# Performance work log

Hardware: AMD Instinct MI355X
Metric: run time of the kernel (lower is better)

## Reference

```python
import jax, jax.numpy as jnp
import numpy as np

D_MODEL = 1024
N_HEAD = 16
D_H = D_MODEL // N_HEAD


def setup_inputs() -> dict:
    key = jax.random.key(0)
    ks = jax.random.split(key, 5)
    scale = 1.0 / np.sqrt(D_MODEL)
    x = jax.random.normal(ks[0], (4, 2048, D_MODEL), dtype=jnp.float32)
    # torch nn.Linear weights: shape (out_features, in_features)
    W_qkv = jax.random.uniform(ks[1], (3 * D_MODEL, D_MODEL), dtype=jnp.float32, minval=-scale, maxval=scale)
    b_qkv = jax.random.uniform(ks[2], (3 * D_MODEL,), dtype=jnp.float32, minval=-scale, maxval=scale)
    W_o = jax.random.uniform(ks[3], (D_MODEL, D_MODEL), dtype=jnp.float32, minval=-scale, maxval=scale)
    b_o = jax.random.uniform(ks[4], (D_MODEL,), dtype=jnp.float32, minval=-scale, maxval=scale)
    return {"x": x, "W_qkv": W_qkv, "b_qkv": b_qkv, "W_o": W_o, "b_o": b_o}


def reference(x, W_qkv, b_qkv, W_o, b_o):
    B, S, D = x.shape
    qkv = jnp.einsum('bsd,ed->bse', x, W_qkv) + b_qkv  # [B,S,3D]
    q, k, v = jnp.split(qkv, 3, axis=-1)
    # [B,H,S,d_h]
    q = q.reshape(B, S, N_HEAD, D_H).transpose(0, 2, 1, 3)
    k = k.reshape(B, S, N_HEAD, D_H).transpose(0, 2, 1, 3)
    v = v.reshape(B, S, N_HEAD, D_H).transpose(0, 2, 1, 3)
    sim = jnp.einsum('bhqd,bhkd->bhqk', q, k) / jnp.sqrt(jnp.float32(D_H))
    neg_inf = jnp.finfo(sim.dtype).min
    causal = jnp.tril(jnp.ones((S, S), dtype=bool))
    sim = jnp.where(causal[None, None], sim, neg_inf)
    attn = jax.nn.softmax(sim, axis=-1)
    out = jnp.einsum('bhqk,bhkd->bhqd', attn, v)  # [B,H,S,d_h]
    out = out.transpose(0, 2, 1, 3).reshape(B, S, D)
    return jnp.einsum('bsd,ed->bse', out, W_o) + b_o
```

## Files before the change

### kernel.cpp

```cpp
#include <hip/hip_runtime.h>

#define D_MODEL 1024
#define S_LEN   2048
#define BATCH   4
#define NH      16
#define DH      64
#define M_ROWS  (BATCH * S_LEN)

typedef __attribute__((ext_vector_type(8))) short short8;
typedef __attribute__((ext_vector_type(4))) float floatx4;
typedef unsigned short ushort_t;
typedef __attribute__((ext_vector_type(4))) ushort_t ushortx4;

__device__ __forceinline__ ushort_t f2bf(float f) {
    union { float f; unsigned u; } v; v.f = f;
    unsigned r = v.u + 0x7FFFu + ((v.u >> 16) & 1u);
    return (ushort_t)(r >> 16);
}

__device__ __forceinline__ int pack2(float lo, float hi) {
    return (int)__builtin_amdgcn_perm(__float_as_uint(hi), __float_as_uint(lo), 0x07060302u);
}

__device__ __forceinline__ void async_copy16(const ushort_t* g, ushort_t* l) {
    __builtin_amdgcn_global_load_lds(
        (const __attribute__((address_space(1))) void*)g,
        (__attribute__((address_space(3))) void*)l,
        16, 0, 0);
}

#define N0 (M_ROWS * D_MODEL)
#define N1 (3 * D_MODEL * D_MODEL)
#define N2 (D_MODEL * D_MODEL)
#define NQUADS ((N0 + N1 + N2) / 4)

__global__ __launch_bounds__(256)
void cvt_f32_bf16(const float* __restrict__ s0, const float* __restrict__ s1,
                  const float* __restrict__ s2, ushort_t* __restrict__ d0,
                  ushort_t* __restrict__ d1, ushort_t* __restrict__ d2)
{
    const int q = blockIdx.x * 256 + threadIdx.x;
    if (q >= NQUADS) return;
    const float* s; ushort_t* d; int e;
    if (q < N0 / 4)            { s = s0; d = d0; e = q * 4; }
    else if (q < (N0 + N1) / 4){ s = s1; d = d1; e = q * 4 - N0; }
    else                       { s = s2; d = d2; e = q * 4 - N0 - N1; }
    const float4 v = *(const float4*)&s[e];
    ushortx4 o;
    o[0] = f2bf(v.x); o[1] = f2bf(v.y); o[2] = f2bf(v.z); o[3] = f2bf(v.w);
    *(ushortx4*)&d[e] = o;
}

template<int BM, int BN, int NWAVES, int MINW, bool F32OUT, bool VSPLIT>
__global__ __launch_bounds__(NWAVES * 64, MINW)
void gemm_bt_bias(const ushort_t* __restrict__ A, const ushort_t* __restrict__ B,
                  const float* __restrict__ bias, void* __restrict__ Cv,
                  ushort_t* __restrict__ vt, int M, int N, int K)
{
    constexpr int BK = 64;
    constexpr int AI = BM / 8 / NWAVES;
    constexpr int BI = BN / 8 / NWAVES;
    constexpr float C2 = 0.18033688011112042f;
    __shared__ ushort_t As[BM][BK];
    __shared__ ushort_t Bs[BN][BK];

    const int tid  = threadIdx.x;
    const int lane = tid & 63;
    const int wave = tid >> 6;
    const int quad = lane >> 4;
    const int l16  = lane & 15;
    const int l8r  = lane >> 3;
    const int c8   = lane & 7;
    const int swz  = l16 & 7;

    const int gdx = gridDim.x;
    const int bid = blockIdx.y * gdx + blockIdx.x;
    const int nwg = gdx * gridDim.y;
    const int sw  = (bid & 7) * (nwg >> 3) + (bid >> 3);
    const int bm  = (sw / gdx) * BM;
    const int bn  = (sw % gdx) * BN;

    const int wm = (wave % (BM / 64)) * 64;
    const int wn = (wave / (BM / 64)) * 64;

    const ushort_t* ag[AI]; ushort_t* al[AI];
    const ushort_t* bg[BI]; ushort_t* bl[BI];
    #pragma unroll
    for (int i = 0; i < AI; i++) {
        const int ri = (wave + i * NWAVES) * 8;
        ag[i] = &A[(size_t)(bm + ri + l8r) * K + (c8 ^ l8r) * 8];
        al[i] = &As[ri][0];
    }
    #pragma unroll
    for (int i = 0; i < BI; i++) {
        const int ri = (wave + i * NWAVES) * 8;
        bg[i] = &B[(size_t)(bn + ri + l8r) * K + (c8 ^ l8r) * 8];
        bl[i] = &Bs[ri][0];
    }

    floatx4 acc[4][4] = {};

    for (int k0 = 0; k0 < K; k0 += BK) {
        __syncthreads();
        #pragma unroll
        for (int i = 0; i < AI; i++) async_copy16(ag[i] + k0, al[i]);
        #pragma unroll
        for (int i = 0; i < BI; i++) async_copy16(bg[i] + k0, bl[i]);
        __syncthreads();

        #pragma unroll
        for (int h = 0; h < 2; h++) {
            short8 af[4], bfr[4];
            #pragma unroll
            for (int i = 0; i < 4; i++)
                af[i]  = *(const short8*)&As[wm + i * 16 + l16][((h * 4 + quad) ^ swz) * 8];
            #pragma unroll
            for (int i = 0; i < 4; i++)
                bfr[i] = *(const short8*)&Bs[wn + i * 16 + l16][((h * 4 + quad) ^ swz) * 8];

            #pragma unroll
            for (int mi = 0; mi < 4; mi++)
                #pragma unroll
                for (int ni = 0; ni < 4; ni++)
                    acc[mi][ni] = __builtin_amdgcn_mfma_f32_16x16x32_bf16(af[mi], bfr[ni], acc[mi][ni], 0, 0, 0);
        }
    }

    #pragma unroll
    for (int ni = 0; ni < 4; ni++) {
        const int col = bn + wn + ni * 16 + l16;
        const float bv = bias[col];
        #pragma unroll
        for (int mi = 0; mi < 4; mi++)
            #pragma unroll
            for (int r = 0; r < 4; r++) {
                const int row = bm + wm + mi * 16 + quad * 4 + r;
                const float val = acc[mi][ni][r] + bv;
                if (VSPLIT) {
                    if (col < 2 * D_MODEL) {
                        const float vv = (col < D_MODEL) ? val * C2 : val;
                        ((ushort_t*)Cv)[(size_t)row * 2048 + col] = f2bf(vv);
                    } else {
                        const int vcol = col - 2 * D_MODEL;
                        const int h = vcol >> 6, dh = vcol & 63;
                        const int b = row >> 11, s = row & 2047;
                        const int sp = (s & ~63) | ((s & 15) << 2) | ((s >> 4) & 3);
                        vt[(((size_t)(b * NH + h)) * DH + dh) * S_LEN + sp] = f2bf(val);
                    }
                } else if (F32OUT) {
                    ((float*)Cv)[(size_t)row * N + col] = val;
                } else {
                    ((ushort_t*)Cv)[(size_t)row * N + col] = f2bf(val);
                }
            }
    }
}

#define BKV 64

struct TileState {
    short8  qf[2];
    floatx4 o[4];
    float   l[4];
};

__device__ __forceinline__ void attn_tile(
    const ushort_t (*__restrict__ Ks)[DH], const ushort_t (*__restrict__ Vs)[BKV],
    ushort_t* __restrict__ Psw, TileState& st, bool diag,
    int wave, int quad, int l16, int swz, short8 ones)
{
    floatx4 sc[4];
    #pragma unroll
    for (int ns = 0; ns < 4; ns++) {
        const short8 kf0 = *(const short8*)&Ks[ns * 16 + l16][(quad ^ swz) * 8];
        const short8 kf1 = *(const short8*)&Ks[ns * 16 + l16][((4 + quad) ^ swz) * 8];
        floatx4 z = {};
        z = __builtin_amdgcn_mfma_f32_16x16x32_bf16(st.qf[0], kf0, z, 0, 0, 0);
        z = __builtin_amdgcn_mfma_f32_16x16x32_bf16(st.qf[1], kf1, z, 0, 0, 0);
        sc[ns] = z;
    }

    #pragma unroll
    for (int r = 0; r < 4; r++) {
        const int qloc = wave * 16 + quad * 4 + r;
        float p[4];
        #pragma unroll
        for (int ns = 0; ns < 4; ns++) {
            float v = sc[ns][r];
            if (diag) {
                const int kj = ns * 16 + l16;
                v = (kj <= qloc) ? v : -1e30f;
            }
            p[ns] = __builtin_amdgcn_exp2f(v);
        }
        int2 w;
        w.x = pack2(p[0], p[1]);
        w.y = pack2(p[2], p[3]);
        const int row = quad * 4 + r;
        *(int2*)((char*)Psw + row * 128 + (((l16 >> 1) ^ (row & 7)) << 4) + ((l16 & 1) << 3)) = w;
    }

    short8 pf[2];
    #pragma unroll
    for (int c = 0; c < 2; c++)
        pf[c] = *(const short8*)((const char*)Psw + l16 * 128 + ((((c << 2) | quad) ^ (l16 & 7)) << 4));

    floatx4 racc = {};
    racc = __builtin_amdgcn_mfma_f32_16x16x32_bf16(pf[0], ones, racc, 0, 0, 0);
    racc = __builtin_amdgcn_mfma_f32_16x16x32_bf16(pf[1], ones, racc, 0, 0, 0);

    #pragma unroll
    for (int r = 0; r < 4; r++)
        st.l[r] += racc[r];

    #pragma unroll
    for (int d = 0; d < 4; d++) {
        #pragma unroll
        for (int c = 0; c < 2; c++) {
            const short8 vf = *(const short8*)&Vs[d * 16 + l16][((c * 4 + quad) ^ swz) * 8];
            st.o[d] = __builtin_amdgcn_mfma_f32_16x16x32_bf16(pf[c], vf, st.o[d], 0, 0, 0);
        }
    }
}

__device__ __forceinline__ void stage_tile(
    const ushort_t* __restrict__ kg, const ushort_t* __restrict__ vg, int kb,
    ushort_t (*__restrict__ Ksb)[DH], ushort_t (*__restrict__ Vsb)[BKV],
    int wave, int l8r, int c8)
{
    #pragma unroll
    for (int i = wave; i < 8; i += 4) {
        const int row = i * 8 + l8r;
        const int cc  = (c8 ^ l8r) * 8;
        async_copy16(&kg[(size_t)(kb + row) * 2048 + cc], &Ksb[i * 8][0]);
        async_copy16(&vg[(size_t)row * S_LEN + kb + cc], &Vsb[i * 8][0]);
    }
}

__global__ __launch_bounds__(256, 4)
void attn_causal(const ushort_t* __restrict__ qk, const ushort_t* __restrict__ vt,
                 ushort_t* __restrict__ out)
{
    __shared__ ushort_t Ks[2][BKV][DH];
    __shared__ ushort_t Vs[2][DH][BKV];
    __shared__ ushort_t Ps[4][16][64];

    const int tid  = threadIdx.x;
    const int lane = tid & 63;
    const int wave = tid >> 6;
    const int quad = lane >> 4;
    const int l16  = lane & 15;
    const int l8r  = lane >> 3;
    const int c8   = lane & 7;
    const int swz  = l16 & 7;

    const int qa = blockIdx.x;
    const int qb = 31 - qa;
    const int bh = blockIdx.y;
    const int b  = bh >> 4;
    const int h  = bh & 15;

    const size_t qkbase = (size_t)b * S_LEN * 2048;
    const ushort_t* kg = qk + qkbase + D_MODEL + h * DH;
    const ushort_t* vg = vt + (size_t)(b * NH + h) * DH * S_LEN;

    TileState sa, sb;
    #pragma unroll
    for (int r = 0; r < 4; r++) { sa.l[r] = 0.f; sb.l[r] = 0.f; }
    #pragma unroll
    for (int d = 0; d < 4; d++) { sa.o[d] = (floatx4){}; sb.o[d] = (floatx4){}; }

    {
        const ushort_t* qpa = qk + qkbase + (size_t)(qa * 64 + wave * 16 + l16) * 2048 + h * DH;
        sa.qf[0] = *(const short8*)(qpa + quad * 8);
        sa.qf[1] = *(const short8*)(qpa + 32 + quad * 8);
        const ushort_t* qpb = qk + qkbase + (size_t)(qb * 64 + wave * 16 + l16) * 2048 + h * DH;
        sb.qf[0] = *(const short8*)(qpb + quad * 8);
        sb.qf[1] = *(const short8*)(qpb + 32 + quad * 8);
    }

    short8 ones;
    #pragma unroll
    for (int j = 0; j < 8; j++) ones[j] = (short)0x3F80;

    stage_tile(kg, vg, 0, Ks[0], Vs[0], wave, l8r, c8);

    int cur = 0;
    for (int t = 0; t <= qb; t++) {
        __syncthreads();
        if (t < qb)
            stage_tile(kg, vg, (t + 1) * BKV, Ks[cur ^ 1], Vs[cur ^ 1], wave, l8r, c8);

        if (t <= qa) attn_tile(Ks[cur], Vs[cur], &Ps[wave][0][0], sa, t == qa, wave, quad, l16, swz, ones);
        attn_tile(Ks[cur], Vs[cur], &Ps[wave][0][0], sb, t == qb, wave, quad, l16, swz, ones);
        cur ^= 1;
    }

    #pragma unroll
    for (int r = 0; r < 4; r++) {
        const float inva = 1.0f / sa.l[r];
        const float invb = 1.0f / sb.l[r];
        const int ra = qa * 64 + wave * 16 + quad * 4 + r;
        const int rb = qb * 64 + wave * 16 + quad * 4 + r;
        #pragma unroll
        for (int d = 0; d < 4; d++) {
            out[(size_t)(b * S_LEN + ra) * D_MODEL + h * DH + d * 16 + l16] = f2bf(sa.o[d][r] * inva);
            out[(size_t)(b * S_LEN + rb) * D_MODEL + h * DH + d * 16 + l16] = f2bf(sb.o[d][r] * invb);
        }
    }
}

extern "C" void kernel_launch(void* const* d_in, const int* in_sizes, int n_in,
                              void* d_out, int out_size, void* d_ws, size_t ws_size,
                              hipStream_t stream)
{
    const float* x    = (const float*)d_in[0];
    const float* Wqkv = (const float*)d_in[1];
    const float* bqkv = (const float*)d_in[2];
    const float* Wo   = (const float*)d_in[3];
    const float* bo   = (const float*)d_in[4];
    float* out = (float*)d_out;

    ushort_t* xb    = (ushort_t*)d_ws;
    ushort_t* wqkvb = xb + N0;
    ushort_t* wob   = wqkvb + N1;
    ushort_t* qkbuf = wob + N2;
    ushort_t* vtbuf = qkbuf + (size_t)M_ROWS * 2048;
    ushort_t* att   = vtbuf + (size_t)BATCH * NH * DH * S_LEN;

    cvt_f32_bf16<<<dim3((NQUADS + 255) / 256), dim3(256), 0, stream>>>(x, Wqkv, Wo, xb, wqkvb, wob);
    gemm_bt_bias<256, 128, 8, 4, false, true>
        <<<dim3((3 * D_MODEL) / 128, M_ROWS / 256), dim3(512), 0, stream>>>(
        xb, wqkvb, bqkv, qkbuf, vtbuf, M_ROWS, 3 * D_MODEL, D_MODEL);
    attn_causal<<<dim3(16, BATCH * NH), dim3(256), 0, stream>>>(qkbuf, vtbuf, att);
    gemm_bt_bias<128, 128, 4, 2, true, false>
        <<<dim3(D_MODEL / 128, M_ROWS / 128), dim3(256), 0, stream>>>(
        att, wob, bo, out, nullptr, M_ROWS, D_MODEL, D_MODEL);
}
```

Measured before the change: 273.1 us.

## Triple-buffer GEMM loads with vmcnt waits, add MFMA priority and attention block swizzle

Replaces the single-buffered GEMM main loop with a three-stage LDS ring. Tiles are prefetched two iterations ahead, and explicit s_waitcnt vmcnt waits replace the double __syncthreads, so global loads overlap MFMA compute. The output projection now uses the same 256x128, 512-thread configuration. The attention kernel raises wave priority around MFMA sections and remaps block IDs for better L2 locality. Tripling LDS for the GEMM (147 KB) limits occupancy and relies on the vmcnt counts matching the issued loads.

Result: no change. 269.2 us (-1.4%).

```diff
diff --git a/kernel.cpp b/kernel.cpp
--- a/kernel.cpp
+++ b/kernel.cpp
@@ -51,18 +51,18 @@
     *(ushortx4*)&d[e] = o;
 }
 
-template<int BM, int BN, int NWAVES, int MINW, bool F32OUT, bool VSPLIT>
-__global__ __launch_bounds__(NWAVES * 64, MINW)
-void gemm_bt_bias(const ushort_t* __restrict__ A, const ushort_t* __restrict__ B,
-                  const float* __restrict__ bias, void* __restrict__ Cv,
-                  ushort_t* __restrict__ vt, int M, int N, int K)
-{
+template<bool F32OUT, bool VSPLIT>
+__global__ __launch_bounds__(512, 2)
+void gemm_pipe(const ushort_t* __restrict__ A, const ushort_t* __restrict__ B,
+               const float* __restrict__ bias, void* __restrict__ Cv,
+               ushort_t* __restrict__ vt, int M, int N, int K)
+{
+    constexpr int BM = 256;
+    constexpr int BN = 128;
     constexpr int BK = 64;
-    constexpr int AI = BM / 8 / NWAVES;
-    constexpr int BI = BN / 8 / NWAVES;
     constexpr float C2 = 0.18033688011112042f;
-    __shared__ ushort_t As[BM][BK];
-    __shared__ ushort_t Bs[BN][BK];
+    __shared__ ushort_t As[3][BM][BK];
+    __shared__ ushort_t Bs[3][BN][BK];
 
     const int tid  = threadIdx.x;
     const int lane = tid & 63;
@@ -80,43 +80,50 @@
     const int bm  = (sw / gdx) * BM;
     const int bn  = (sw % gdx) * BN;
 
-    const int wm = (wave % (BM / 64)) * 64;
-    const int wn = (wave / (BM / 64)) * 64;
-
-    const ushort_t* ag[AI]; ushort_t* al[AI];
-    const ushort_t* bg[BI]; ushort_t* bl[BI];
-    #pragma unroll
-    for (int i = 0; i < AI; i++) {
-        const int ri = (wave + i * NWAVES) * 8;
-        ag[i] = &A[(size_t)(bm + ri + l8r) * K + (c8 ^ l8r) * 8];
-        al[i] = &As[ri][0];
-    }
-    #pragma unroll
-    for (int i = 0; i < BI; i++) {
-        const int ri = (wave + i * NWAVES) * 8;
-        bg[i] = &B[(size_t)(bn + ri + l8r) * K + (c8 ^ l8r) * 8];
-        bl[i] = &Bs[ri][0];
-    }
+    const int wm = (wave & 3) * 64;
+    const int wn = (wave >> 2) * 64;
+
+    const int NT = K >> 6;
+
+    auto STAGE = [&](int s, int kt) {
+        const int k0 = kt * BK;
+        const int cc = (c8 ^ l8r) * 8;
+        #pragma unroll
+        for (int i = 0; i < 4; i++) {
+            const int rb = (i * 8 + wave) * 8;
+            async_copy16(&A[(size_t)(bm + rb + l8r) * K + k0 + cc], &As[s][rb][0]);
+        }
+        #pragma unroll
+        for (int i = 0; i < 2; i++) {
+            const int rb = (i * 8 + wave) * 8;
+            async_copy16(&B[(size_t)(bn + rb + l8r) * K + k0 + cc], &Bs[s][rb][0]);
+        }
+    };
+
+    STAGE(0, 0);
+    STAGE(1, 1);
 
     floatx4 acc[4][4] = {};
 
-    for (int k0 = 0; k0 < K; k0 += BK) {
-        __syncthreads();
-        #pragma unroll
-        for (int i = 0; i < AI; i++) async_copy16(ag[i] + k0, al[i]);
-        #pragma unroll
-        for (int i = 0; i < BI; i++) async_copy16(bg[i] + k0, bl[i]);
-        __syncthreads();
-
+    for (int t = 0; t < NT; t++) {
+        if (t + 1 < NT) {
+            asm volatile("s_waitcnt vmcnt(6)" ::: "memory");
+        } else {
+            asm volatile("s_waitcnt vmcnt(0)" ::: "memory");
+        }
+        __builtin_amdgcn_s_barrier();
+        if (t + 2 < NT) STAGE((t + 2) % 3, t + 2);
+
+        const int s = t % 3;
         #pragma unroll
         for (int h = 0; h < 2; h++) {
             short8 af[4], bfr[4];
             #pragma unroll
             for (int i = 0; i < 4; i++)
-                af[i]  = *(const short8*)&As[wm + i * 16 + l16][((h * 4 + quad) ^ swz) * 8];
+                af[i]  = *(const short8*)&As[s][wm + i * 16 + l16][((h * 4 + quad) ^ swz) * 8];
             #pragma unroll
             for (int i = 0; i < 4; i++)
-                bfr[i] = *(const short8*)&Bs[wn + i * 16 + l16][((h * 4 + quad) ^ swz) * 8];
+                bfr[i] = *(const short8*)&Bs[s][wn + i * 16 + l16][((h * 4 + quad) ^ swz) * 8];
 
             #pragma unroll
             for (int mi = 0; mi < 4; mi++)
@@ -143,8 +150,8 @@
                     } else {
                         const int vcol = col - 2 * D_MODEL;
                         const int h = vcol >> 6, dh = vcol & 63;
-                        const int b = row >> 11, s = row & 2047;
-                        const int sp = (s & ~63) | ((s & 15) << 2) | ((s >> 4) & 3);
+                        const int b = row >> 11, s2 = row & 2047;
+                        const int sp = (s2 & ~63) | ((s2 & 15) << 2) | ((s2 >> 4) & 3);
                         vt[(((size_t)(b * NH + h)) * DH + dh) * S_LEN + sp] = f2bf(val);
                     }
                 } else if (F32OUT) {
@@ -170,6 +177,7 @@
     int wave, int quad, int l16, int swz, short8 ones)
 {
     floatx4 sc[4];
+    __builtin_amdgcn_s_setprio(1);
     #pragma unroll
     for (int ns = 0; ns < 4; ns++) {
         const short8 kf0 = *(const short8*)&Ks[ns * 16 + l16][(quad ^ swz) * 8];
@@ -179,6 +187,7 @@
         z = __builtin_amdgcn_mfma_f32_16x16x32_bf16(st.qf[1], kf1, z, 0, 0, 0);
         sc[ns] = z;
     }
+    __builtin_amdgcn_s_setprio(0);
 
     #pragma unroll
     for (int r = 0; r < 4; r++) {
@@ -205,6 +214,7 @@
     for (int c = 0; c < 2; c++)
         pf[c] = *(const short8*)((const char*)Psw + l16 * 128 + ((((c << 2) | quad) ^ (l16 & 7)) << 4));
 
+    __builtin_amdgcn_s_setprio(1);
     floatx4 racc = {};
     racc = __builtin_amdgcn_mfma_f32_16x16x32_bf16(pf[0], ones, racc, 0, 0, 0);
     racc = __builtin_amdgcn_mfma_f32_16x16x32_bf16(pf[1], ones, racc, 0, 0, 0);
@@ -221,6 +231,7 @@
             st.o[d] = __builtin_amdgcn_mfma_f32_16x16x32_bf16(pf[c], vf, st.o[d], 0, 0, 0);
         }
     }
+    __builtin_amdgcn_s_setprio(0);
 }
 
 __device__ __forceinline__ void stage_tile(
@@ -254,11 +265,13 @@
     const int c8   = lane & 7;
     const int swz  = l16 & 7;
 
-    const int qa = blockIdx.x;
-    const int qb = 31 - qa;
-    const int bh = blockIdx.y;
-    const int b  = bh >> 4;
-    const int h  = bh & 15;
+    const int id  = blockIdx.y * 16 + blockIdx.x;
+    const int sid = (id & 7) * 128 + (id >> 3);
+    const int qa  = sid & 15;
+    const int qb  = 31 - qa;
+    const int bh  = sid >> 4;
+    const int b   = bh >> 4;
+    const int h   = bh & 15;
 
     const size_t qkbase = (size_t)b * S_LEN * 2048;
     const ushort_t* kg = qk + qkbase + D_MODEL + h * DH;
@@ -329,11 +342,11 @@
     ushort_t* att   = vtbuf + (size_t)BATCH * NH * DH * S_LEN;
 
     cvt_f32_bf16<<<dim3((NQUADS + 255) / 256), dim3(256), 0, stream>>>(x, Wqkv, Wo, xb, wqkvb, wob);
-    gemm_bt_bias<256, 128, 8, 4, false, true>
+    gemm_pipe<false, true>
         <<<dim3((3 * D_MODEL) / 128, M_ROWS / 256), dim3(512), 0, stream>>>(
         xb, wqkvb, bqkv, qkbuf, vtbuf, M_ROWS, 3 * D_MODEL, D_MODEL);
     attn_causal<<<dim3(16, BATCH * NH), dim3(256), 0, stream>>>(qkbuf, vtbuf, att);
-    gemm_bt_bias<128, 128, 4, 2, true, false>
-        <<<dim3(D_MODEL / 128, M_ROWS / 128), dim3(256), 0, stream>>>(
+    gemm_pipe<true, false>
+        <<<dim3(D_MODEL / 128, M_ROWS / 256), dim3(512), 0, stream>>>(
         att, wob, bo, out, nullptr, M_ROWS, D_MODEL, D_MODEL);
 }
```
